# Performance work log

Measured on AMD Instinct MI355X. Metric: run time of the kernel, lower is better.

## Reference

```python
import jax, jax.numpy as jnp
import numpy as np

B, L, D = 1, 4096, 2048
H, KVH, HD = 8, 2, 256
WINDOW = 512
BASE = 10000.0
ROPE_FRACTION = 1.0


def _rms_norm(x, scale=None):
    x32 = x.astype(jnp.float32)
    var = jnp.mean(jnp.square(x32), axis=-1, keepdims=True)
    xn = x32 * jax.lax.rsqrt(var + 1e-6)
    return xn if scale is None else xn * scale.astype(jnp.float32)


def _apply_rope(x, positions, base, rope_fraction):
    head_dim = x.shape[-1]
    rope_dim = int(head_dim * rope_fraction)
    if rope_dim == 0:
        return x
    half = rope_dim // 2
    head_half = head_dim // 2
    freq_exp = 2.0 * jnp.arange(half, dtype=jnp.float32) / head_dim
    timescale = base ** freq_exp
    pos = positions[..., None].astype(jnp.float32)          # [B, L, 1]
    sinusoid = pos / timescale[None, None, :]               # [B, L, half]
    sin = jnp.sin(sinusoid)[:, :, None, :]                  # [B, L, 1, half]
    cos = jnp.cos(sinusoid)[:, :, None, :]
    x1 = x[..., :half]
    x2 = x[..., head_half:head_half + half]
    x1r = x1 * cos - x2 * sin
    x2r = x2 * cos + x1 * sin
    if rope_dim == head_dim:
        return jnp.concatenate([x1r, x2r], axis=-1)
    return jnp.concatenate(
        [x1r, x[..., half:head_half], x2r, x[..., head_half + half:]], axis=-1)


def setup_inputs() -> dict:
    key = jax.random.key(0)
    ks = jax.random.split(key, 5)
    x = jax.random.normal(ks[0], (B, L, D), dtype=jnp.float32)
    positions = jnp.broadcast_to(jnp.arange(L, dtype=jnp.int32)[None, :], (B, L))
    s = 0.02
    Wq = jax.random.normal(ks[1], (D, H * HD), dtype=jnp.float32) * s
    Wk = jax.random.normal(ks[2], (D, KVH * HD), dtype=jnp.float32) * s
    Wv = jax.random.normal(ks[3], (D, KVH * HD), dtype=jnp.float32) * s
    Wo = jax.random.normal(ks[4], (H * HD, D), dtype=jnp.float32) * s
    q_scale = jnp.ones((HD,), dtype=jnp.float32)
    k_scale = jnp.ones((HD,), dtype=jnp.float32)
    return {"x": x, "positions": positions, "Wq": Wq, "Wk": Wk, "Wv": Wv,
            "Wo": Wo, "q_scale": q_scale, "k_scale": k_scale}


def reference(x, positions, Wq, Wk, Wv, Wo, q_scale, k_scale):
    # projections (no bias, no 1/sqrt(d) scaling, matching the source)
    q = (x @ Wq).reshape(B, L, H, HD)
    k = (x @ Wk).reshape(B, L, KVH, HD)
    v = (x @ Wv).reshape(B, L, KVH, HD)
    # QK RMSNorm (learned scale), V RMSNorm (no scale)
    q = _apply_rope(_rms_norm(q, q_scale), positions, BASE, ROPE_FRACTION)
    k = _apply_rope(_rms_norm(k, k_scale), positions, BASE, ROPE_FRACTION)
    v = _rms_norm(v)
    # GQA head repeat
    rep = H // KVH
    k = jnp.repeat(k, rep, axis=2)  # [B, L, H, HD]
    v = jnp.repeat(v, rep, axis=2)
    # attention scores [B, H, Lq, Lk]
    scores = jnp.einsum('bqhd,bkhd->bhqk', q, k)
    qi = jnp.arange(L)[:, None]
    kj = jnp.arange(L)[None, :]
    mask = (kj <= qi) & (kj >= qi - WINDOW + 1)  # causal & sliding window
    scores = jnp.where(mask[None, None, :, :], scores, -10000.0)
    probs = jax.nn.softmax(scores.astype(jnp.float32), axis=-1)
    out = jnp.einsum('bhqk,bkhd->bqhd', probs, v)
    return out.reshape(B, L, H * HD) @ Wo
```

## Files before the change

kernel.cpp:

```cpp
#include <hip/hip_runtime.h>
#include <hip/hip_bf16.h>
#include <math.h>
#include <stdint.h>

#define L_      4096
#define D_      2048
#define H_      8
#define KVH_    2
#define HD_     256
#define WINDOW_ 512
#define QKVW    3072

typedef __attribute__((ext_vector_type(8))) _Float16 f16x8;
typedef __attribute__((ext_vector_type(4))) _Float16 f16x4;
typedef __attribute__((ext_vector_type(4))) short s16x4;
typedef __attribute__((ext_vector_type(4))) float f32x4;

__device__ __forceinline__ short f2h(float f) {
    _Float16 h = (_Float16)f;
    return *reinterpret_cast<short*>(&h);
}
__device__ __forceinline__ float h2f(short s) {
    _Float16 h = *reinterpret_cast<_Float16*>(&s);
    return (float)h;
}

__device__ __forceinline__ void gl2lds16(const void* g, void* l) {
    __builtin_amdgcn_global_load_lds(
        (const __attribute__((address_space(1))) uint32_t*)g,
        (__attribute__((address_space(3))) uint32_t*)l, 16, 0, 0);
}

__global__ __launch_bounds__(256) void cast_f16(const float* __restrict__ X,
                                                short* __restrict__ Y, int n) {
    int idx = (blockIdx.x * 256 + threadIdx.x) * 8;
    if (idx >= n) return;
    float4 a = *(const float4*)(X + idx);
    float4 b = *(const float4*)(X + idx + 4);
    s16x4 o0, o1;
    o0[0]=f2h(a.x); o0[1]=f2h(a.y); o0[2]=f2h(a.z); o0[3]=f2h(a.w);
    o1[0]=f2h(b.x); o1[1]=f2h(b.y); o1[2]=f2h(b.z); o1[3]=f2h(b.w);
    *(s16x4*)(Y + idx)     = o0;
    *(s16x4*)(Y + idx + 4) = o1;
}

__global__ __launch_bounds__(256) void transpose_cast(const float* __restrict__ W,
                                                      short* __restrict__ Wt,
                                                      int K, int N) {
    __shared__ float tl[32][33];
    int t = threadIdx.x;
    int c = t & 31, r4 = (t >> 5) * 4;
    int k0 = blockIdx.y * 32, n0 = blockIdx.x * 32;
#pragma unroll
    for (int i = 0; i < 4; ++i)
        tl[r4 + i][c] = W[(size_t)(k0 + r4 + i) * N + n0 + c];
    __syncthreads();
#pragma unroll
    for (int i = 0; i < 4; ++i)
        Wt[(size_t)(n0 + r4 + i) * K + k0 + c] = f2h(tl[c][r4 + i]);
}

template <int OUT_HALF>
__global__ __launch_bounds__(256) void gemm_mfma(const short* __restrict__ A,
                                                 const short* __restrict__ Bt,
                                                 void* __restrict__ Cout,
                                                 int M, int N, int K) {
    __shared__ short As[128][64];
    __shared__ short Bs[128][64];

    const int tid = threadIdx.x;
    const int w = tid >> 6, lane = tid & 63;
    const int lq = lane & 15, quad = lane >> 4;
    const int bm = blockIdx.y * 128, bn = blockIdx.x * 128;
    const int wm = (w & 1) * 64, wn = (w >> 1) * 64;
    const int lrow = lane >> 3;
    const int slot = lane & 7;

    f32x4 acc[4][4];
#pragma unroll
    for (int i = 0; i < 4; ++i)
#pragma unroll
        for (int j = 0; j < 4; ++j) acc[i][j] = 0;

    for (int k0 = 0; k0 < K; k0 += 64) {
#pragma unroll
        for (int c = 0; c < 4; ++c) {
            const int r0 = w * 32 + c * 8;
            const int row = r0 + lrow;
            const int chunk = slot ^ (row & 7);
            gl2lds16(A  + (size_t)(bm + row) * K + k0 + chunk * 8, &As[r0][0]);
            gl2lds16(Bt + (size_t)(bn + row) * K + k0 + chunk * 8, &Bs[r0][0]);
        }
        __syncthreads();

#pragma unroll
        for (int f = 0; f < 2; ++f) {
            const int sA = (((f * 4) + quad) ^ (lq & 7)) * 8;
            f16x8 af[4], bfr[4];
#pragma unroll
            for (int i = 0; i < 4; ++i) af[i]  = *(const f16x8*)&As[wm + i * 16 + lq][sA];
#pragma unroll
            for (int j = 0; j < 4; ++j) bfr[j] = *(const f16x8*)&Bs[wn + j * 16 + lq][sA];
#pragma unroll
            for (int i = 0; i < 4; ++i)
#pragma unroll
                for (int j = 0; j < 4; ++j)
                    acc[i][j] = __builtin_amdgcn_mfma_f32_16x16x32_f16(af[i], bfr[j], acc[i][j], 0, 0, 0);
        }
        __syncthreads();
    }

#pragma unroll
    for (int i = 0; i < 4; ++i)
#pragma unroll
        for (int r = 0; r < 4; ++r) {
            int row = bm + wm + i * 16 + quad * 4 + r;
#pragma unroll
            for (int j = 0; j < 4; ++j) {
                int col = bn + wn + j * 16 + lq;
                float v = acc[i][j][r];
                if (OUT_HALF) ((short*)Cout)[(size_t)row * N + col] = f2h(v);
                else          ((float*)Cout)[(size_t)row * N + col] = v;
            }
        }
}

__global__ __launch_bounds__(256) void norm_rope_h(short* __restrict__ qkv,
                                                   const float* __restrict__ q_scale,
                                                   const float* __restrict__ k_scale,
                                                   const int* __restrict__ positions) {
    const int row = blockIdx.x;
    const int token = row / 12, ridx = row % 12;
    short* p = qkv + (size_t)token * QKVW + ridx * HD_;
    const int d = threadIdx.x;

    float val = h2f(p[d]);
    float ss = val * val;
#pragma unroll
    for (int off = 32; off > 0; off >>= 1) ss += __shfl_down(ss, off);
    __shared__ float wss[4];
    __shared__ float xs[HD_];
    if ((d & 63) == 0) wss[d >> 6] = ss;
    __syncthreads();
    const float var = (wss[0] + wss[1] + wss[2] + wss[3]) * (1.0f / (float)HD_);
    float xn = val * rsqrtf(var + 1e-6f);
    if (ridx < 8)       xn *= q_scale[d];
    else if (ridx < 10) xn *= k_scale[d];

    if (ridx >= 10) { p[d] = f2h(xn); return; }

    xs[d] = xn;
    __syncthreads();
    const int pos = positions[token];
    const int i = d & 127;
    const float fe = (float)(2 * i) * (1.0f / (float)HD_);
    const float inv_ts = __expf(fe * -9.210340371976184f);
    const float ang = (float)pos * inv_ts;
    float s, c;
    __sincosf(ang, &s, &c);
    float outv = (d < 128) ? (xn * c - xs[d + 128] * s)
                           : (xn * c + xs[d - 128] * s);
    p[d] = f2h(outv);
}

__global__ __launch_bounds__(256) void vt_prep(const short* __restrict__ qkv,
                                               short* __restrict__ vtg) {
    const int tok0 = blockIdx.x * 64;
    const int g = blockIdx.y;
    const int tid = threadIdx.x;
    __shared__ short Vs[64][264];
#pragma unroll
    for (int i = 0; i < 8; ++i) {
        int f = (tid + i * 256) * 8;
        int tok = f >> 8, d = f & 255;
        *(int4*)&Vs[tok][d] =
            *(const int4*)(qkv + (size_t)(tok0 + tok) * QKVW + 2560 + g * HD_ + d);
    }
    __syncthreads();
    const int d = tid;
    short tmp[64];
#pragma unroll
    for (int j = 0; j < 64; ++j) tmp[j] = Vs[j][d];
    short* dst = vtg + ((size_t)g * HD_ + d) * L_ + tok0;
#pragma unroll
    for (int c = 0; c < 8; ++c)
        *(int4*)(dst + c * 8) = *(const int4*)&tmp[c * 8];
}

__global__ __launch_bounds__(256) void attn_mfma(const short* __restrict__ qkv,
                                                 const short* __restrict__ vtg,
                                                 short* __restrict__ ao) {
    const int bx = blockIdx.x;
    const int g = bx & 1, qt = bx >> 1;
    const int q0 = qt * 16;
    const int tid = threadIdx.x;
    const int w = tid >> 6, lane = tid & 63;
    const int lq = lane & 15, quad = lane >> 4;
    const int h = g * 4 + w;

    __shared__ short lds[18688];
    short (*Ks)[264] = (short (*)[264])lds;
    short (*Vt)[40]  = (short (*)[40])(lds + 8448);

    f16x8 qf[8];
    {
        const short* qrow = qkv + (size_t)(q0 + lq) * QKVW + h * HD_;
#pragma unroll
        for (int f = 0; f < 8; ++f)
            qf[f] = *(const f16x8*)(qrow + f * 32 + quad * 8);
    }

    float m_run = -INFINITY, l_run = 0.0f;

    f32x4 accO[16];
#pragma unroll
    for (int dt = 0; dt < 16; ++dt) accO[dt] = 0;

    const short* kcol = qkv + 2048 + g * HD_;
    const short* vrow = vtg + (size_t)g * HD_ * L_;
    const int qi = q0 + lq;

    for (int kt = 0; kt < 17; ++kt) {
        const int kbase = q0 - WINDOW_ + kt * 32;
        if (kbase + 32 <= 0) continue;

        {
            const int row = tid >> 3;
            const int co = (tid & 7) * 32;
            int kj = kbase + row;
            kj = min(max(kj, 0), L_ - 1);
            const short* src = kcol + (size_t)kj * QKVW + co;
            short* dst = &Ks[row][co];
#pragma unroll
            for (int u = 0; u < 4; ++u)
                *(int4*)(dst + u * 8) = *(const int4*)(src + u * 8);
        }
        {
            const short* src = vrow + (size_t)tid * L_;
#pragma unroll
            for (int c = 0; c < 4; ++c) {
                int ck = kbase + c * 8;
                ck = min(max(ck, 0), L_ - 8);
                *(int4*)&Vt[tid][c * 8] = *(const int4*)(src + ck);
            }
        }
        __syncthreads();

        f32x4 st0 = 0, st1 = 0;
#pragma unroll
        for (int f = 0; f < 8; ++f) {
            f16x8 kf0 = *(const f16x8*)&Ks[lq][f * 32 + quad * 8];
            f16x8 kf1 = *(const f16x8*)&Ks[16 + lq][f * 32 + quad * 8];
            st0 = __builtin_amdgcn_mfma_f32_16x16x32_f16(kf0, qf[f], st0, 0, 0, 0);
            st1 = __builtin_amdgcn_mfma_f32_16x16x32_f16(kf1, qf[f], st1, 0, 0, 0);
        }

        const int kA = kbase + quad * 4;
        const int kB = kA + 16;
        float sv[8]; bool vd[8];
#pragma unroll
        for (int r = 0; r < 4; ++r) {
            int ka = kA + r, kb = kB + r;
            vd[r]     = (ka >= 0) && (ka <= qi) && (ka > qi - WINDOW_);
            vd[4 + r] = (kb >= 0) && (kb <= qi) && (kb > qi - WINDOW_);
            sv[r]     = vd[r]     ? st0[r] : -INFINITY;
            sv[4 + r] = vd[4 + r] ? st1[r] : -INFINITY;
        }
        float mt = sv[0];
#pragma unroll
        for (int i = 1; i < 8; ++i) mt = fmaxf(mt, sv[i]);
        mt = fmaxf(mt, __shfl_xor(mt, 16));
        mt = fmaxf(mt, __shfl_xor(mt, 32));
        const float mn = fmaxf(m_run, mt);
        const float alpha = (mn == -INFINITY) ? 1.0f : __expf(m_run - mn);
        float pv[8], rs = 0.0f;
#pragma unroll
        for (int i = 0; i < 8; ++i) {
            pv[i] = vd[i] ? __expf(sv[i] - mn) : 0.0f;
            rs += pv[i];
        }
        rs += __shfl_xor(rs, 16);
        rs += __shfl_xor(rs, 32);
        m_run = mn;
        l_run = l_run * alpha + rs;

        f16x4 p0, p1;
#pragma unroll
        for (int i = 0; i < 4; ++i) { p0[i] = (_Float16)pv[i]; p1[i] = (_Float16)pv[4 + i]; }

#pragma unroll
        for (int dt = 0; dt < 16; ++dt) {
            f16x4 v0 = *(const f16x4*)&Vt[dt * 16 + lq][quad * 4];
            f16x4 v1 = *(const f16x4*)&Vt[dt * 16 + lq][16 + quad * 4];
            f32x4 t = accO[dt];
#pragma unroll
            for (int r = 0; r < 4; ++r) t[r] *= alpha;
            t = __builtin_amdgcn_mfma_f32_16x16x16f16(v0, p0, t, 0, 0, 0);
            t = __builtin_amdgcn_mfma_f32_16x16x16f16(v1, p1, t, 0, 0, 0);
            accO[dt] = t;
        }
        __syncthreads();
    }

    const float inv = 1.0f / l_run;
    short* myE = lds + w * 4224;
#pragma unroll
    for (int dt = 0; dt < 16; ++dt) {
        f16x4 e;
#pragma unroll
        for (int r = 0; r < 4; ++r) e[r] = (_Float16)(accO[dt][r] * inv);
        *(f16x4*)&myE[lq * 264 + dt * 16 + quad * 4] = e;
    }
    {
        const int row = lane >> 2;
        const int c0 = (lane & 3) * 64;
        short* orow = ao + (size_t)(q0 + row) * 2048 + h * HD_ + c0;
#pragma unroll
        for (int u = 0; u < 8; ++u)
            *(int4*)(orow + u * 8) = *(const int4*)&myE[row * 264 + c0 + u * 8];
    }
}

extern "C" void kernel_launch(void* const* d_in, const int* in_sizes, int n_in,
                              void* d_out, int out_size, void* d_ws, size_t ws_size,
                              hipStream_t stream) {
    const float* x         = (const float*)d_in[0];
    const int*   positions = (const int*)d_in[1];
    const float* Wq        = (const float*)d_in[2];
    const float* Wk        = (const float*)d_in[3];
    const float* Wv        = (const float*)d_in[4];
    const float* Wo        = (const float*)d_in[5];
    const float* q_scale   = (const float*)d_in[6];
    const float* k_scale   = (const float*)d_in[7];
    float*       out       = (float*)d_out;

    char* ws = (char*)d_ws;
    short* xb    = (short*)(ws);
    short* qkv   = (short*)(ws + 16777216);
    short* ao    = (short*)(ws + 41943040);
    short* Wtqkv = (short*)(ws + 58720256);
    short* Wto   = (short*)(ws + 71303168);
    short* vtg   = xb;

    cast_f16<<<4096, 256, 0, stream>>>(x, xb, L_ * D_);
    transpose_cast<<<dim3(2048 / 32, 2048 / 32), 256, 0, stream>>>(Wq, Wtqkv, D_, 2048);
    transpose_cast<<<dim3(512 / 32, 2048 / 32), 256, 0, stream>>>(Wk, Wtqkv + (size_t)2048 * D_, D_, 512);
    transpose_cast<<<dim3(512 / 32, 2048 / 32), 256, 0, stream>>>(Wv, Wtqkv + (size_t)2560 * D_, D_, 512);
    transpose_cast<<<dim3(2048 / 32, 2048 / 32), 256, 0, stream>>>(Wo, Wto, 2048, 2048);

    gemm_mfma<1><<<dim3(QKVW / 128, L_ / 128), 256, 0, stream>>>(xb, Wtqkv, qkv, L_, QKVW, D_);

    norm_rope_h<<<L_ * 12, 256, 0, stream>>>(qkv, q_scale, k_scale, positions);

    vt_prep<<<dim3(L_ / 64, KVH_), 256, 0, stream>>>(qkv, vtg);

    attn_mfma<<<(L_ / 16) * KVH_, 256, 0, stream>>>(qkv, vtg, ao);

    gemm_mfma<0><<<dim3(D_ / 128, L_ / 128), 256, 0, stream>>>(ao, Wto, out, L_, D_, 2048);
}
```

Measured before the change: 340.1 us.

## Add 256x256-tile pipelined MFMA GEMM for QKV projection

Adds a new GEMM kernel for the QKV projection that uses 256x256 output tiles, 512 threads and double-buffered LDS. Tiles are loaded directly into LDS with an XOR swizzle, and the workgroup order is swizzled. Loads for the next K-step are interleaved with MFMA phases using barriers, waitcnt and setprio. The aim is more data reuse per tile and better overlap of memory traffic with matrix math. The trade-off is high register and LDS use (128KB LDS), and the grid shrinks to 192 workgroups, which may underfill the GPU.

```diff
diff --git a/kernel.cpp b/kernel.cpp
--- a/kernel.cpp
+++ b/kernel.cpp
@@ -119,6 +119,127 @@
             for (int j = 0; j < 4; ++j) {
                 int col = bn + wn + j * 16 + lq;
                 float v = acc[i][j][r];
+                if (OUT_HALF) ((short*)Cout)[(size_t)row * N + col] = f2h(v);
+                else          ((float*)Cout)[(size_t)row * N + col] = v;
+            }
+        }
+}
+
+template <int OUT_HALF>
+__global__ __launch_bounds__(512, 2) void gemm_mfma256(const short* __restrict__ A,
+                                                       const short* __restrict__ Bt,
+                                                       void* __restrict__ Cout,
+                                                       int M, int N, int K) {
+    __shared__ short As[2][256][64];
+    __shared__ short Bs[2][256][64];
+
+    const int tid = threadIdx.x;
+    const int w = tid >> 6, lane = tid & 63;
+    const int lq = lane & 15, quad = lane >> 4;
+    const int lq7 = lq & 7;
+    const int wm128 = (w >> 2) * 128;
+    const int wn = (w & 3) * 64;
+
+    int bid = blockIdx.y * gridDim.x + blockIdx.x;
+    int nwg = gridDim.x * gridDim.y;
+    int qch = nwg >> 3;
+    int swz = (bid & 7) * qch + (bid >> 3);
+    const int bn = (swz % gridDim.x) * 256;
+    const int bm = (swz / gridDim.x) * 256;
+
+    const int KT = K >> 6, KTm1 = KT - 1;
+
+    auto stageA = [&](int s, int kt2, int mq) {
+        const int k0 = min(kt2, KTm1) * 64;
+#pragma unroll
+        for (int i = 0; i < 2; ++i) {
+            const int r0 = i * 128 + mq * 64 + w * 8;
+            const int row = r0 + (lane >> 3);
+            const int chunk = (lane & 7) ^ (row & 7);
+            gl2lds16(A + (size_t)(bm + row) * K + k0 + chunk * 8, &As[s][r0][0]);
+        }
+    };
+    auto stageB = [&](int s, int kt2, int nq) {
+        const int k0 = min(kt2, KTm1) * 64;
+#pragma unroll
+        for (int i = 0; i < 2; ++i) {
+            const int g = i * 2 + (w >> 2);
+            const int r0 = g * 64 + nq * 32 + (w & 3) * 8;
+            const int row = r0 + (lane >> 3);
+            const int chunk = (lane & 7) ^ (row & 7);
+            gl2lds16(Bt + (size_t)(bn + row) * K + k0 + chunk * 8, &Bs[s][r0][0]);
+        }
+    };
+
+    f32x4 acc[8][4];
+#pragma unroll
+    for (int i = 0; i < 8; ++i)
+#pragma unroll
+        for (int j = 0; j < 4; ++j) acc[i][j] = 0;
+
+    f16x8 af[4][2];
+    f16x8 bf[2][2];
+
+#define QPHASE(S, MQ, NQ, READA, STAGE_STMT)                                     \
+    do {                                                                         \
+        if (READA) {                                                             \
+            _Pragma("unroll") for (int i_ = 0; i_ < 4; ++i_)                     \
+            _Pragma("unroll") for (int ks_ = 0; ks_ < 2; ++ks_)                  \
+                af[i_][ks_] = *(const f16x8*)&As[S][wm128 + (MQ)*64 + i_*16 + lq]\
+                                                   [((ks_*4 + quad) ^ lq7) * 8]; \
+        }                                                                        \
+        _Pragma("unroll") for (int j_ = 0; j_ < 2; ++j_)                         \
+        _Pragma("unroll") for (int ks_ = 0; ks_ < 2; ++ks_)                      \
+            bf[j_][ks_] = *(const f16x8*)&Bs[S][wn + (NQ)*32 + j_*16 + lq]       \
+                                               [((ks_*4 + quad) ^ lq7) * 8];     \
+        STAGE_STMT;                                                              \
+        asm volatile("s_waitcnt vmcnt(6)" ::: "memory");                         \
+        __builtin_amdgcn_s_barrier();                                            \
+        asm volatile("s_waitcnt lgkmcnt(0)" ::: "memory");                       \
+        __builtin_amdgcn_sched_barrier(0);                                       \
+        __builtin_amdgcn_s_setprio(1);                                           \
+        _Pragma("unroll") for (int i_ = 0; i_ < 4; ++i_)                         \
+        _Pragma("unroll") for (int j_ = 0; j_ < 2; ++j_) {                       \
+            acc[(MQ)*4 + i_][(NQ)*2 + j_] = __builtin_amdgcn_mfma_f32_16x16x32_f16( \
+                af[i_][0], bf[j_][0], acc[(MQ)*4 + i_][(NQ)*2 + j_], 0, 0, 0);   \
+            acc[(MQ)*4 + i_][(NQ)*2 + j_] = __builtin_amdgcn_mfma_f32_16x16x32_f16( \
+                af[i_][1], bf[j_][1], acc[(MQ)*4 + i_][(NQ)*2 + j_], 0, 0, 0);   \
+        }                                                                        \
+        __builtin_amdgcn_s_setprio(0);                                           \
+        __builtin_amdgcn_s_barrier();                                            \
+    } while (0)
+
+    stageA(0, 0, 0);
+    stageB(0, 0, 0);
+    stageB(0, 0, 1);
+    stageA(0, 0, 1);
+    stageA(1, 1, 0);
+    asm volatile("s_waitcnt vmcnt(6)" ::: "memory");
+    __builtin_amdgcn_s_barrier();
+
+    for (int kt = 0; kt < KT; kt += 2) {
+        QPHASE(0, 0, 0, true,  stageB(1, kt + 1, 0));
+        QPHASE(0, 0, 1, false, stageB(1, kt + 1, 1));
+        QPHASE(0, 1, 0, true,  stageA(1, kt + 1, 1));
+        QPHASE(0, 1, 1, false, stageA(0, kt + 2, 0));
+        QPHASE(1, 0, 0, true,  stageB(0, kt + 2, 0));
+        QPHASE(1, 0, 1, false, stageB(0, kt + 2, 1));
+        QPHASE(1, 1, 0, true,  stageA(0, kt + 2, 1));
+        QPHASE(1, 1, 1, false, stageA(1, kt + 3, 0));
+    }
+#undef QPHASE
+
+    asm volatile("s_waitcnt vmcnt(0)" ::: "memory");
+
+#pragma unroll
+    for (int mi = 0; mi < 8; ++mi)
+#pragma unroll
+        for (int r = 0; r < 4; ++r) {
+            int row = bm + wm128 + mi * 16 + quad * 4 + r;
+#pragma unroll
+            for (int j = 0; j < 4; ++j) {
+                int col = bn + wn + j * 16 + lq;
+                float v = acc[mi][j][r];
                 if (OUT_HALF) ((short*)Cout)[(size_t)row * N + col] = f2h(v);
                 else          ((float*)Cout)[(size_t)row * N + col] = v;
             }
@@ -348,7 +469,7 @@
     transpose_cast<<<dim3(512 / 32, 2048 / 32), 256, 0, stream>>>(Wv, Wtqkv + (size_t)2560 * D_, D_, 512);
     transpose_cast<<<dim3(2048 / 32, 2048 / 32), 256, 0, stream>>>(Wo, Wto, 2048, 2048);
 
-    gemm_mfma<1><<<dim3(QKVW / 128, L_ / 128), 256, 0, stream>>>(xb, Wtqkv, qkv, L_, QKVW, D_);
+    gemm_mfma256<1><<<dim3(QKVW / 256, L_ / 256), 512, 0, stream>>>(xb, Wtqkv, qkv, L_, QKVW, D_);
 
     norm_rope_h<<<L_ * 12, 256, 0, stream>>>(qkv, q_scale, k_scale, positions);
 
```

After: 342.7 us. No clear change (+0.8%).
